# Kernel optimization log

Measured on AMD Instinct MI355X. Metric: run time of the kernel, lower is better.

Reference implementation:

```python
import math
import jax, jax.numpy as jnp
import numpy as np

B, L, DM, D, C = 8, 2048, 512, 512, 2
K_TOP = int(math.floor(C * math.log(L)))  # floor(c * log L) = 15


def setup_inputs() -> dict:
    key = jax.random.key(0)
    ks = jax.random.split(key, 9)
    s = 0.02
    return {
        "Q": jax.random.normal(ks[0], (B, L, DM), jnp.float32),
        "K": jax.random.normal(ks[1], (B, L, DM), jnp.float32),
        "V": jax.random.normal(ks[2], (B, L, DM), jnp.float32),
        "WQ_w": jax.random.normal(ks[3], (DM, D), jnp.float32) * s,
        "WQ_b": jnp.zeros((D,), jnp.float32),
        "WK_w": jax.random.normal(ks[4], (DM, D), jnp.float32) * s,
        "WK_b": jnp.zeros((D,), jnp.float32),
        "WV_w": jax.random.normal(ks[5], (DM, D), jnp.float32) * s,
        "WV_b": jnp.zeros((D,), jnp.float32),
    }


def reference(Q, K, V, WQ_w, WQ_b, WK_w, WK_b, WV_w, WV_b):
    Bn, Ln, _ = Q.shape
    # K/V truncated (zero-padded if shorter) to length L; here S == L.
    Kc = K[:, :Ln, :]
    Vc = V[:, :Ln, :]
    # Dense projections
    q = Q @ WQ_w + WQ_b    # [B, L, d]
    k = Kc @ WK_w + WK_b   # [B, L, d]
    v = Vc @ WV_w + WV_b   # [B, L, d]
    # FFT-based autocorrelation along the time axis
    Qf = jnp.fft.rfft(q, axis=1)
    Kf = jnp.fft.rfft(k, axis=1)
    Rxx = jnp.fft.irfft(Qf * jnp.conjugate(Kf), n=Ln, axis=1)  # [B, L, d]
    # Top-k lag selection per (batch, channel)
    Rl = jnp.moveaxis(Rxx, 1, -1)                # [B, d, L]
    Wk, Ik = jax.lax.top_k(Rl, K_TOP)            # [B, d, k]
    Wk = jax.nn.softmax(Wk, axis=-1)
    # Weighted aggregation of time-rolled values: roll(v, -i)[t] = v[(t+i) % L]
    vl = jnp.moveaxis(v, 1, -1)                  # [B, d, L]
    t = jnp.arange(Ln)
    idx = (t[None, None, None, :] + Ik[..., None]) % Ln   # [B, d, k, L]
    rolled = jnp.take_along_axis(vl[:, :, None, :], idx, axis=-1)  # [B, d, k, L]
    A = jnp.einsum('bdk,bdkl->bld', Wk, rolled)  # [B, L, d]
    return A
```

## Files before the change

kernel.cpp:

```cpp
#include <hip/hip_runtime.h>
#include <hip/hip_bf16.h>
#include <math.h>

#define Bz 8
#define Lz 2048
#define Dz 512
#define KTOP 15

typedef __attribute__((ext_vector_type(8))) unsigned short ushort8x;
typedef __attribute__((ext_vector_type(8))) _Float16 half8x;
typedef __attribute__((ext_vector_type(4))) float floatx4;
typedef __attribute__((ext_vector_type(16))) float float16x;

__global__ __launch_bounds__(256) void wtrans3(
    const float* __restrict__ w0, const float* __restrict__ w1,
    const float* __restrict__ w2, _Float16* __restrict__ t0,
    _Float16* __restrict__ t1, _Float16* __restrict__ t2) {
  const float* w = blockIdx.z == 0 ? w0 : (blockIdx.z == 1 ? w1 : w2);
  _Float16* t = blockIdx.z == 0 ? t0 : (blockIdx.z == 1 ? t1 : t2);
  __shared__ float tile[32][33];
  const int n0 = blockIdx.x * 32, k0 = blockIdx.y * 32;
  const int tx = threadIdx.x, ty = threadIdx.y;
  #pragma unroll
  for (int i = 0; i < 4; ++i)
    tile[ty + 8 * i][tx] = w[(size_t)(k0 + ty + 8 * i) * Dz + n0 + tx];
  __syncthreads();
  #pragma unroll
  for (int i = 0; i < 4; ++i)
    t[(size_t)(n0 + ty + 8 * i) * Dz + k0 + tx] = (_Float16)tile[tx][ty + 8 * i];
}

#define GLDA 40
__global__ __launch_bounds__(256) void gemm3(
    const float* __restrict__ A0, const float* __restrict__ A1,
    const float* __restrict__ A2, const _Float16* __restrict__ B0,
    const _Float16* __restrict__ B1, const _Float16* __restrict__ B2,
    const float* __restrict__ c0, const float* __restrict__ c1,
    const float* __restrict__ c2, _Float16* __restrict__ o0,
    _Float16* __restrict__ o1, _Float16* __restrict__ o2) {
  const int K = Dz;
  const int z = blockIdx.z;
  const float* A = z == 0 ? A0 : (z == 1 ? A1 : A2);
  const _Float16* Bt = z == 0 ? B0 : (z == 1 ? B1 : B2);
  const float* bias = z == 0 ? c0 : (z == 1 ? c1 : c2);
  _Float16* oT = z == 0 ? o0 : (z == 1 ? o1 : o2);

  __shared__ _Float16 smem[20480];
  _Float16* Asb = smem;
  _Float16* Bsb = smem + 10240;
  const int tid = threadIdx.x;
  const int m0 = blockIdx.y * 128;
  const int n0 = blockIdx.x * 128;
  const int lane = tid & 63;
  const int wv = tid >> 6;
  const int wr = wv & 1, wc = wv >> 1;
  const int ln = lane & 15;
  const int quad = lane >> 4;

  floatx4 acc[4][4];
  #pragma unroll
  for (int i = 0; i < 4; ++i)
    #pragma unroll
    for (int j = 0; j < 4; ++j) acc[i][j] = (floatx4){0.f, 0.f, 0.f, 0.f};

  float4 ra4[4];
  ushort8x rb[2];

  #pragma unroll
  for (int j = 0; j < 4; ++j) {
    const int slot = tid + 256 * j;
    const int r = slot >> 3, c4 = slot & 7;
    ra4[j] = *(const float4*)&A[(size_t)(m0 + r) * K + 4 * c4];
  }
  #pragma unroll
  for (int j = 0; j < 2; ++j) {
    const int slot = tid + 256 * j;
    const int r = slot >> 2, ch = slot & 3;
    rb[j] = *(const ushort8x*)((const unsigned short*)Bt +
                               (size_t)(n0 + r) * K + 8 * ch);
  }
  {
    _Float16* As = Asb;
    _Float16* Bs = Bsb;
    #pragma unroll
    for (int j = 0; j < 4; ++j) {
      const int slot = tid + 256 * j;
      const int r = slot >> 3, c4 = slot & 7;
      union { _Float16 h[4]; unsigned long long u; } p;
      p.h[0] = (_Float16)ra4[j].x;
      p.h[1] = (_Float16)ra4[j].y;
      p.h[2] = (_Float16)ra4[j].z;
      p.h[3] = (_Float16)ra4[j].w;
      *(unsigned long long*)&As[r * GLDA + 4 * c4] = p.u;
    }
    #pragma unroll
    for (int j = 0; j < 2; ++j) {
      const int slot = tid + 256 * j;
      const int r = slot >> 2, ch = slot & 3;
      *(ushort8x*)&Bs[r * GLDA + 8 * ch] = rb[j];
    }
  }
  __syncthreads();

  const int NKT = K / 32;
  for (int kt = 0; kt < NKT; ++kt) {
    const int cur = kt & 1;
    if (kt + 1 < NKT) {
      const int kof = (kt + 1) * 32;
      #pragma unroll
      for (int j = 0; j < 4; ++j) {
        const int slot = tid + 256 * j;
        const int r = slot >> 3, c4 = slot & 7;
        ra4[j] = *(const float4*)&A[(size_t)(m0 + r) * K + kof + 4 * c4];
      }
      #pragma unroll
      for (int j = 0; j < 2; ++j) {
        const int slot = tid + 256 * j;
        const int r = slot >> 2, ch = slot & 3;
        rb[j] = *(const ushort8x*)((const unsigned short*)Bt +
                                   (size_t)(n0 + r) * K + kof + 8 * ch);
      }
    }
    const _Float16* As = Asb + cur * 5120;
    const _Float16* Bs = Bsb + cur * 5120;
    half8x af[4], bf[4];
    #pragma unroll
    for (int i = 0; i < 4; ++i)
      af[i] = *(const half8x*)&As[(wr * 64 + 16 * i + ln) * GLDA + 8 * quad];
    #pragma unroll
    for (int j = 0; j < 4; ++j)
      bf[j] = *(const half8x*)&Bs[(wc * 64 + 16 * j + ln) * GLDA + 8 * quad];
    #pragma unroll
    for (int i = 0; i < 4; ++i)
      #pragma unroll
      for (int j = 0; j < 4; ++j)
        acc[i][j] = __builtin_amdgcn_mfma_f32_16x16x32_f16(af[i], bf[j], acc[i][j], 0, 0, 0);
    if (kt + 1 < NKT) {
      const int nxt = cur ^ 1;
      _Float16* Asw = Asb + nxt * 5120;
      _Float16* Bsw = Bsb + nxt * 5120;
      #pragma unroll
      for (int j = 0; j < 4; ++j) {
        const int slot = tid + 256 * j;
        const int r = slot >> 3, c4 = slot & 7;
        union { _Float16 h[4]; unsigned long long u; } p;
        p.h[0] = (_Float16)ra4[j].x;
        p.h[1] = (_Float16)ra4[j].y;
        p.h[2] = (_Float16)ra4[j].z;
        p.h[3] = (_Float16)ra4[j].w;
        *(unsigned long long*)&Asw[r * GLDA + 4 * c4] = p.u;
      }
      #pragma unroll
      for (int j = 0; j < 2; ++j) {
        const int slot = tid + 256 * j;
        const int r = slot >> 2, ch = slot & 3;
        *(ushort8x*)&Bsw[r * GLDA + 8 * ch] = rb[j];
      }
      __syncthreads();
    }
  }

  __syncthreads();
  _Float16* TB = smem;
  #pragma unroll
  for (int j = 0; j < 4; ++j) {
    const int n_l = wc * 64 + 16 * j + ln;
    const float bv = bias[n0 + n_l];
    #pragma unroll
    for (int i = 0; i < 4; ++i) {
      const int m_l = wr * 64 + 16 * i + 4 * quad;
      union { _Float16 h[4]; unsigned long long u; } p;
      #pragma unroll
      for (int r = 0; r < 4; ++r) p.h[r] = (_Float16)(acc[i][j][r] + bv);
      *(unsigned long long*)&TB[n_l * 136 + m_l] = p.u;
    }
  }
  __syncthreads();
  const int b = m0 >> 11;
  const int l0 = m0 & 2047;
  #pragma unroll
  for (int it = 0; it < 8; ++it) {
    const int s = tid + 256 * it;
    const int n = s >> 4, c = s & 15;
    *(ushort8x*)(oT + ((size_t)(b * Dz + n0 + n)) * Lz + l0 + 8 * c) =
        *(const ushort8x*)&TB[n * 136 + 8 * c];
  }
}

#define QXS 2072

__device__ __forceinline__ int swz128(int byte) {
  return byte ^ (((byte >> 7) & 7) << 4);
}

__global__ __launch_bounds__(256) void corr_mfma_topk(
    const _Float16* __restrict__ qT, const _Float16* __restrict__ kT,
    float* __restrict__ Wk, int* __restrict__ Ik) {
  __shared__ __attribute__((aligned(16))) unsigned short qx[8 * QXS];
  __shared__ __attribute__((aligned(16))) unsigned short ke[Lz];
  __shared__ float cv[64];
  __shared__ int ci[64];

  const int tid = threadIdx.x;
  const size_t chan = (size_t)blockIdx.x * Lz;
  const unsigned short* qg = (const unsigned short*)(qT + chan);
  const unsigned short* kg = (const unsigned short*)(kT + chan);

  {
    ushort8x v = *(const ushort8x*)(kg + 8 * tid);
    *(ushort8x*)((char*)ke + swz128(16 * tid)) = v;
  }
  for (int c = tid; c < QXS / 8; c += 256) {
    union { unsigned int d[8]; ushort8x v[2]; } b;
    b.v[0] = *(const ushort8x*)(qg + ((8 * c) & (Lz - 1)));
    b.v[1] = *(const ushort8x*)(qg + ((8 * c + 8) & (Lz - 1)));
    #pragma unroll
    for (int s = 0; s < 8; ++s) {
      union { unsigned int d[4]; ushort8x v; } w;
      if (s & 1) {
        #pragma unroll
        for (int t = 0; t < 4; ++t)
          w.d[t] = __builtin_amdgcn_alignbit(b.d[(s >> 1) + t + 1],
                                             b.d[(s >> 1) + t], 16);
      } else {
        #pragma unroll
        for (int t = 0; t < 4; ++t) w.d[t] = b.d[(s >> 1) + t];
      }
      *(ushort8x*)&qx[s * QXS + 8 * c] = w.v;
    }
  }
  __syncthreads();

  const int lane = tid & 63;
  const int wv = tid >> 6;
  const int jb = lane & 31;
  const int hi = lane >> 5;
  const char* aptr = (const char*)qx + (jb & 7) * (2 * QXS) + 16 * (jb >> 3) + 16 * hi;
  const int bb2 = ((8 * hi - 32 * jb) & (Lz - 1)) * 2;

  float16x acc0 = {0.f, 0.f, 0.f, 0.f, 0.f, 0.f, 0.f, 0.f,
                   0.f, 0.f, 0.f, 0.f, 0.f, 0.f, 0.f, 0.f};
  float16x acc1 = acc0;

  const int t0base = wv << 9;
  #pragma unroll 4
  for (int it = 0; it < 32; ++it) {
    const int t2 = 2 * (t0base + 16 * it);
    half8x a = *(const half8x*)(aptr + t2);
    const int y0 = (bb2 + t2) & (2 * Lz - 1);
    const int y1 = (y0 + 2048) & (2 * Lz - 1);
    half8x b0 = *(const half8x*)((const char*)ke + swz128(y0));
    half8x b1 = *(const half8x*)((const char*)ke + swz128(y1));
    acc0 = __builtin_amdgcn_mfma_f32_32x32x16_f16(a, b0, acc0, 0, 0, 0);
    acc1 = __builtin_amdgcn_mfma_f32_32x32x16_f16(a, b1, acc1, 0, 0, 0);
  }

  __syncthreads();
  float* red = (float*)qx;
  {
    const int rbase = wv * 8192;
    #pragma unroll
    for (int g = 0; g < 4; ++g) {
      const int tau0 = 8 * g + 4 * hi + 32 * jb;
      float4 p0, p1;
      p0.x = acc0[4 * g + 0]; p0.y = acc0[4 * g + 1];
      p0.z = acc0[4 * g + 2]; p0.w = acc0[4 * g + 3];
      p1.x = acc1[4 * g + 0]; p1.y = acc1[4 * g + 1];
      p1.z = acc1[4 * g + 2]; p1.w = acc1[4 * g + 3];
      *(float4*)((char*)red + swz128(rbase + 4 * tau0)) = p0;
      *(float4*)((char*)red + swz128(rbase + 4 * (tau0 + 1024))) = p1;
    }
  }
  __syncthreads();

  float vals[8] = {0.f, 0.f, 0.f, 0.f, 0.f, 0.f, 0.f, 0.f};
  {
    const char* rb = (const char*)red;
    #pragma unroll
    for (int w = 0; w < 4; ++w) {
      float4 a0 = *(const float4*)(rb + swz128(w * 8192 + 32 * tid));
      float4 a1 = *(const float4*)(rb + swz128(w * 8192 + 32 * tid + 16));
      vals[0] += a0.x; vals[1] += a0.y; vals[2] += a0.z; vals[3] += a0.w;
      vals[4] += a1.x; vals[5] += a1.y; vals[6] += a1.z; vals[7] += a1.w;
    }
  }

  unsigned key[8];
  #pragma unroll
  for (int j = 0; j < 8; ++j) {
    const unsigned u = __float_as_uint(vals[j]);
    key[j] = u ^ (unsigned)(((int)u >> 31) | 0x80000000);
  }
  unsigned p = 0;
  for (int b = 31; b >= 0; --b) {
    const unsigned c = p | (1u << b);
    int cnt = 0;
    #pragma unroll
    for (int j = 0; j < 8; ++j)
      cnt += __popcll(__ballot(key[j] >= c));
    if (cnt >= KTOP) p = c;
  }
  const unsigned long long ltm = (1ull << lane) - 1ull;
  int base = 0;
  #pragma unroll
  for (int j = 0; j < 8; ++j) {
    const bool g = key[j] > p;
    const unsigned long long m = __ballot(g);
    const int pos = base + __popcll(m & ltm);
    if (g) { cv[wv * KTOP + pos] = vals[j]; ci[wv * KTOP + pos] = 8 * tid + j; }
    base += __popcll(m);
  }
  #pragma unroll
  for (int j = 0; j < 8; ++j) {
    const bool e = (key[j] == p);
    const unsigned long long m = __ballot(e);
    const int pos = base + __popcll(m & ltm);
    if (e && pos < KTOP) { cv[wv * KTOP + pos] = vals[j]; ci[wv * KTOP + pos] = 8 * tid + j; }
    base += __popcll(m);
  }
  __syncthreads();

  if (wv == 0) {
    const bool act = lane < 4 * KTOP;
    const float v = act ? cv[lane] : 0.f;
    const int ti = act ? ci[lane] : 0;
    unsigned k2 = 0;
    if (act) {
      const unsigned u = __float_as_uint(v);
      k2 = u ^ (unsigned)(((int)u >> 31) | 0x80000000);
    }
    unsigned pp = 0;
    for (int b = 31; b >= 0; --b) {
      const unsigned c = pp | (1u << b);
      if (__popcll(__ballot(k2 >= c)) >= KTOP) pp = c;
    }
    const unsigned long long mg = __ballot(k2 > pp);
    const int tot = __popcll(mg);
    bool sel = (k2 > pp);
    int pos = __popcll(mg & ltm);
    const unsigned long long me = __ballot(k2 == pp);
    const int pose = tot + __popcll(me & ltm);
    if (k2 == pp && pose < KTOP) { sel = true; pos = pose; }
    if (sel) { cv[pos] = v; ci[pos] = ti; }
    const float sv = (lane < KTOP) ? cv[lane] : -3.0e38f;
    const int si = (lane < KTOP) ? ci[lane] : 0;
    float gm = sv;
    #pragma unroll
    for (int off = 1; off < 64; off <<= 1)
      gm = fmaxf(gm, __shfl_xor(gm, off, 64));
    float e = (lane < KTOP) ? expf(sv - gm) : 0.f;
    float es = e;
    #pragma unroll
    for (int off = 1; off < 64; off <<= 1) es += __shfl_xor(es, off, 64);
    if (lane < KTOP) {
      const size_t ob = (size_t)blockIdx.x * KTOP;
      Wk[ob + lane] = e / es;
      Ik[ob + lane] = si;
    }
  }
}

#define GSWZ(b) ((b) ^ ((((b) >> 12) & 7) << 4))

__global__ __launch_bounds__(256) void gather_fused(
    const _Float16* __restrict__ vT, const float* __restrict__ Wk,
    const int* __restrict__ Ik, float* __restrict__ out) {
  __shared__ __attribute__((aligned(16))) _Float16 ls[8 * Lz];
  __shared__ float os[256 * 9];
  const int tid = threadIdx.x;
  const int d0 = blockIdx.x * 8;
  const int b = blockIdx.y;
  float* ob = out + (size_t)b * Lz * Dz;

  const char* lsb = (const char*)ls;
  #pragma unroll
  for (int it = 0; it < 8; ++it) {
    const int slot = tid + 256 * it;
    const int dl2 = slot >> 8, c = slot & 255;
    ushort8x v = *(const ushort8x*)((const unsigned short*)vT +
                                    ((size_t)(b * Dz + d0 + dl2) * Lz) + 8 * c);
    *(ushort8x*)((char*)ls + GSWZ(16 * slot)) = v;
  }

  const int dl = tid & 7;
  const int lg = tid >> 3;
  const size_t wb = ((size_t)b * Dz + d0 + dl) * KTOP;
  float wreg[KTOP];
  int ireg[KTOP];
  #pragma unroll
  for (int k = 0; k < KTOP; ++k) {
    wreg[k] = Wk[wb + k];
    ireg[k] = Ik[wb + k];
  }
  __syncthreads();

  const int rowb = dl * 4096;
  for (int lt = 0; lt < 8; ++lt) {
    const int lbase = lt * 256 + lg * 8;
    float acc[8] = {0.f, 0.f, 0.f, 0.f, 0.f, 0.f, 0.f, 0.f};
    for (int k = 0; k < KTOP; ++k) {
      const float w = wreg[k];
      const int p = (lbase + ireg[k]) & (Lz - 1);
      const int b0 = p >> 3;
      const int b1 = (b0 + 1) & 255;
      union { ushort8x v; unsigned d[4]; } A0, A1;
      A0.v = *(const ushort8x*)(lsb + GSWZ(rowb + 16 * b0));
      A1.v = *(const ushort8x*)(lsb + GSWZ(rowb + 16 * b1));
      const int h = p & 7;
      unsigned e0, e1, e2, e3, e4, e5;
      if (h & 4) { e0 = A0.d[2]; e1 = A0.d[3]; e2 = A1.d[0]; e3 = A1.d[1]; e4 = A1.d[2]; e5 = A1.d[3]; }
      else       { e0 = A0.d[0]; e1 = A0.d[1]; e2 = A0.d[2]; e3 = A0.d[3]; e4 = A1.d[0]; e5 = A1.d[1]; }
      unsigned f0, f1, f2, f3, f4;
      if (h & 2) { f0 = e1; f1 = e2; f2 = e3; f3 = e4; f4 = e5; }
      else       { f0 = e0; f1 = e1; f2 = e2; f3 = e3; f4 = e4; }
      const int sh = (h & 1) << 4;
      unsigned o0 = __builtin_amdgcn_alignbit(f1, f0, sh);
      unsigned o1 = __builtin_amdgcn_alignbit(f2, f1, sh);
      unsigned o2 = __builtin_amdgcn_alignbit(f3, f2, sh);
      unsigned o3 = __builtin_amdgcn_alignbit(f4, f3, sh);
      union { unsigned u; _Float16 hh[2]; } c0, c1, c2, c3;
      c0.u = o0; c1.u = o1; c2.u = o2; c3.u = o3;
      acc[0] += w * (float)c0.hh[0]; acc[1] += w * (float)c0.hh[1];
      acc[2] += w * (float)c1.hh[0]; acc[3] += w * (float)c1.hh[1];
      acc[4] += w * (float)c2.hh[0]; acc[5] += w * (float)c2.hh[1];
      acc[6] += w * (float)c3.hh[0]; acc[7] += w * (float)c3.hh[1];
    }
    __syncthreads();
    #pragma unroll
    for (int j = 0; j < 8; ++j) os[(lg * 8 + j) * 9 + dl] = acc[j];
    __syncthreads();
    #pragma unroll
    for (int c2 = 0; c2 < 2; ++c2) {
      const int sl = tid + 256 * c2;
      const int l = sl >> 1, c = sl & 1;
      float4 o;
      o.x = os[l * 9 + 4 * c + 0];
      o.y = os[l * 9 + 4 * c + 1];
      o.z = os[l * 9 + 4 * c + 2];
      o.w = os[l * 9 + 4 * c + 3];
      *(float4*)&ob[(size_t)(lt * 256 + l) * Dz + d0 + 4 * c] = o;
    }
  }
}

extern "C" void kernel_launch(void* const* d_in, const int* in_sizes, int n_in,
                              void* d_out, int out_size, void* d_ws, size_t ws_size,
                              hipStream_t stream) {
  const float* Q = (const float*)d_in[0];
  const float* K = (const float*)d_in[1];
  const float* V = (const float*)d_in[2];
  const float* WQw = (const float*)d_in[3];
  const float* WQb = (const float*)d_in[4];
  const float* WKw = (const float*)d_in[5];
  const float* WKb = (const float*)d_in[6];
  const float* WVw = (const float*)d_in[7];
  const float* WVb = (const float*)d_in[8];
  float* out = (float*)d_out;

  const size_t CH = (size_t)Bz * Dz;
  const size_t NEL = (size_t)Bz * Lz * Dz;

  char* ws = (char*)d_ws;
  _Float16* qT = (_Float16*)ws;
  _Float16* kT = qT + NEL;
  _Float16* vT = kT + NEL;
  _Float16* WQt = vT + NEL;
  _Float16* WKt = WQt + (size_t)Dz * Dz;
  _Float16* WVt = WKt + (size_t)Dz * Dz;
  float* Wk = (float*)(WVt + (size_t)Dz * Dz);
  int* Ik = (int*)(Wk + CH * KTOP);

  dim3 tr_block(32, 8);

  wtrans3<<<dim3(16, 16, 3), tr_block, 0, stream>>>(WQw, WKw, WVw, WQt, WKt, WVt);

  gemm3<<<dim3(Dz / 128, (Bz * Lz) / 128, 3), dim3(256), 0, stream>>>(
      Q, K, V, WQt, WKt, WVt, WQb, WKb, WVb, qT, kT, vT);

  corr_mfma_topk<<<dim3((unsigned)CH), dim3(256), 0, stream>>>(qT, kT, Wk, Ik);

  gather_fused<<<dim3(Dz / 8, Bz), dim3(256), 0, stream>>>(vT, Wk, Ik, out);
}
```

Baseline: 269.1 us.

## Load GEMM B tiles directly into LDS and drop LDS-staged epilogue

The projection GEMM now fetches the fp16 transposed weight tiles with global_load_lds into an unpadded, XOR-swizzled LDS layout. This removes the register round trip and the separate LDS stores for B, and shrinks shared memory. The epilogue no longer transposes through LDS with extra barriers. Each lane now writes 8-byte fp16 chunks straight to the transposed output, which saves LDS traffic and syncs but makes the global writes narrower and less coalesced.

After: 272.1 us. About the same (+1.1%).

```diff
diff --git a/kernel.cpp b/kernel.cpp
--- a/kernel.cpp
+++ b/kernel.cpp
@@ -30,7 +30,7 @@
     t[(size_t)(n0 + ty + 8 * i) * Dz + k0 + tx] = (_Float16)tile[tx][ty + 8 * i];
 }
 
-#define GLDA 40
+#define ALDA 40
 __global__ __launch_bounds__(256) void gemm3(
     const float* __restrict__ A0, const float* __restrict__ A1,
     const float* __restrict__ A2, const _Float16* __restrict__ B0,
@@ -45,7 +45,7 @@
   const float* bias = z == 0 ? c0 : (z == 1 ? c1 : c2);
   _Float16* oT = z == 0 ? o0 : (z == 1 ? o1 : o2);
 
-  __shared__ _Float16 smem[20480];
+  __shared__ __attribute__((aligned(16))) _Float16 smem[18432];
   _Float16* Asb = smem;
   _Float16* Bsb = smem + 10240;
   const int tid = threadIdx.x;
@@ -64,7 +64,6 @@
     for (int j = 0; j < 4; ++j) acc[i][j] = (floatx4){0.f, 0.f, 0.f, 0.f};
 
   float4 ra4[4];
-  ushort8x rb[2];
 
   #pragma unroll
   for (int j = 0; j < 4; ++j) {
@@ -73,38 +72,34 @@
     ra4[j] = *(const float4*)&A[(size_t)(m0 + r) * K + 4 * c4];
   }
   #pragma unroll
-  for (int j = 0; j < 2; ++j) {
+  for (int jj = 0; jj < 2; ++jj) {
+    const int s = tid + 256 * jj;
+    const int row = s >> 2;
+    const int qs = (s & 3) ^ (row & 3);
+    const unsigned short* src =
+        (const unsigned short*)Bt + (size_t)(n0 + row) * K + 8 * qs;
+    __builtin_amdgcn_global_load_lds(
+        (const __attribute__((address_space(1))) unsigned int*)src,
+        (__attribute__((address_space(3))) unsigned int*)&Bsb[(jj * 256 + wv * 64) * 8],
+        16, 0, 0);
+  }
+  #pragma unroll
+  for (int j = 0; j < 4; ++j) {
     const int slot = tid + 256 * j;
-    const int r = slot >> 2, ch = slot & 3;
-    rb[j] = *(const ushort8x*)((const unsigned short*)Bt +
-                               (size_t)(n0 + r) * K + 8 * ch);
-  }
-  {
-    _Float16* As = Asb;
-    _Float16* Bs = Bsb;
-    #pragma unroll
-    for (int j = 0; j < 4; ++j) {
-      const int slot = tid + 256 * j;
-      const int r = slot >> 3, c4 = slot & 7;
-      union { _Float16 h[4]; unsigned long long u; } p;
-      p.h[0] = (_Float16)ra4[j].x;
-      p.h[1] = (_Float16)ra4[j].y;
-      p.h[2] = (_Float16)ra4[j].z;
-      p.h[3] = (_Float16)ra4[j].w;
-      *(unsigned long long*)&As[r * GLDA + 4 * c4] = p.u;
-    }
-    #pragma unroll
-    for (int j = 0; j < 2; ++j) {
-      const int slot = tid + 256 * j;
-      const int r = slot >> 2, ch = slot & 3;
-      *(ushort8x*)&Bs[r * GLDA + 8 * ch] = rb[j];
-    }
+    const int r = slot >> 3, c4 = slot & 7;
+    union { _Float16 h[4]; unsigned long long u; } p;
+    p.h[0] = (_Float16)ra4[j].x;
+    p.h[1] = (_Float16)ra4[j].y;
+    p.h[2] = (_Float16)ra4[j].z;
+    p.h[3] = (_Float16)ra4[j].w;
+    *(unsigned long long*)&Asb[r * ALDA + 4 * c4] = p.u;
   }
   __syncthreads();
 
   const int NKT = K / 32;
   for (int kt = 0; kt < NKT; ++kt) {
     const int cur = kt & 1;
+    const int nxt = cur ^ 1;
     if (kt + 1 < NKT) {
       const int kof = (kt + 1) * 32;
       #pragma unroll
@@ -114,31 +109,37 @@
         ra4[j] = *(const float4*)&A[(size_t)(m0 + r) * K + kof + 4 * c4];
       }
       #pragma unroll
-      for (int j = 0; j < 2; ++j) {
-        const int slot = tid + 256 * j;
-        const int r = slot >> 2, ch = slot & 3;
-        rb[j] = *(const ushort8x*)((const unsigned short*)Bt +
-                                   (size_t)(n0 + r) * K + kof + 8 * ch);
+      for (int jj = 0; jj < 2; ++jj) {
+        const int s = tid + 256 * jj;
+        const int row = s >> 2;
+        const int qs = (s & 3) ^ (row & 3);
+        const unsigned short* src =
+            (const unsigned short*)Bt + (size_t)(n0 + row) * K + kof + 8 * qs;
+        __builtin_amdgcn_global_load_lds(
+            (const __attribute__((address_space(1))) unsigned int*)src,
+            (__attribute__((address_space(3))) unsigned int*)
+                &Bsb[nxt * 4096 + (jj * 256 + wv * 64) * 8],
+            16, 0, 0);
       }
     }
     const _Float16* As = Asb + cur * 5120;
-    const _Float16* Bs = Bsb + cur * 5120;
+    const _Float16* Bs = Bsb + cur * 4096;
     half8x af[4], bf[4];
     #pragma unroll
     for (int i = 0; i < 4; ++i)
-      af[i] = *(const half8x*)&As[(wr * 64 + 16 * i + ln) * GLDA + 8 * quad];
-    #pragma unroll
-    for (int j = 0; j < 4; ++j)
-      bf[j] = *(const half8x*)&Bs[(wc * 64 + 16 * j + ln) * GLDA + 8 * quad];
+      af[i] = *(const half8x*)&As[(wr * 64 + 16 * i + ln) * ALDA + 8 * quad];
+    #pragma unroll
+    for (int j = 0; j < 4; ++j) {
+      const int row = wc * 64 + 16 * j + ln;
+      bf[j] = *(const half8x*)&Bs[row * 32 + 8 * (quad ^ (ln & 3))];
+    }
     #pragma unroll
     for (int i = 0; i < 4; ++i)
       #pragma unroll
       for (int j = 0; j < 4; ++j)
         acc[i][j] = __builtin_amdgcn_mfma_f32_16x16x32_f16(af[i], bf[j], acc[i][j], 0, 0, 0);
     if (kt + 1 < NKT) {
-      const int nxt = cur ^ 1;
       _Float16* Asw = Asb + nxt * 5120;
-      _Float16* Bsw = Bsb + nxt * 5120;
       #pragma unroll
       for (int j = 0; j < 4; ++j) {
         const int slot = tid + 256 * j;
@@ -148,42 +149,26 @@
         p.h[1] = (_Float16)ra4[j].y;
         p.h[2] = (_Float16)ra4[j].z;
         p.h[3] = (_Float16)ra4[j].w;
-        *(unsigned long long*)&Asw[r * GLDA + 4 * c4] = p.u;
-      }
-      #pragma unroll
-      for (int j = 0; j < 2; ++j) {
-        const int slot = tid + 256 * j;
-        const int r = slot >> 2, ch = slot & 3;
-        *(ushort8x*)&Bsw[r * GLDA + 8 * ch] = rb[j];
+        *(unsigned long long*)&Asw[r * ALDA + 4 * c4] = p.u;
       }
       __syncthreads();
     }
   }
 
-  __syncthreads();
-  _Float16* TB = smem;
+  const int bb = m0 >> 11;
+  const int l0 = m0 & 2047;
   #pragma unroll
   for (int j = 0; j < 4; ++j) {
-    const int n_l = wc * 64 + 16 * j + ln;
-    const float bv = bias[n0 + n_l];
+    const int d = n0 + wc * 64 + 16 * j + ln;
+    const float bv = bias[d];
+    _Float16* op = oT + (size_t)(bb * Dz + d) * Lz + l0 + wr * 64 + 4 * quad;
     #pragma unroll
     for (int i = 0; i < 4; ++i) {
-      const int m_l = wr * 64 + 16 * i + 4 * quad;
       union { _Float16 h[4]; unsigned long long u; } p;
       #pragma unroll
       for (int r = 0; r < 4; ++r) p.h[r] = (_Float16)(acc[i][j][r] + bv);
-      *(unsigned long long*)&TB[n_l * 136 + m_l] = p.u;
-    }
-  }
-  __syncthreads();
-  const int b = m0 >> 11;
-  const int l0 = m0 & 2047;
-  #pragma unroll
-  for (int it = 0; it < 8; ++it) {
-    const int s = tid + 256 * it;
-    const int n = s >> 4, c = s & 15;
-    *(ushort8x*)(oT + ((size_t)(b * Dz + n0 + n)) * Lz + l0 + 8 * c) =
-        *(const ushort8x*)&TB[n * 136 + 8 * c];
+      *(unsigned long long*)(op + 16 * i) = p.u;
+    }
   }
 }
 
```

## Deepen gemm3 global-load prefetch to two stages with lightweight barriers

Applied to the files above, without the earlier changes.

The projection GEMM now keeps two K-tiles of global loads in flight in registers, issuing loads for tile kt+2 right after the MFMAs of tile kt. The shared-memory write for tile kt+1 then uses data loaded an iteration earlier. The __syncthreads is replaced with an explicit lgkmcnt wait, sched_barrier and s_barrier. Launch bounds now request 4 waves per SIMD. The aim is to hide global-load latency, at the cost of more live registers, which may spill or cut occupancy under the new bound.

Result: slower. 450.6 us (+67.4%).

```diff
diff --git a/kernel.cpp b/kernel.cpp
--- a/kernel.cpp
+++ b/kernel.cpp
@@ -31,7 +31,7 @@
 }
 
 #define GLDA 40
-__global__ __launch_bounds__(256) void gemm3(
+__global__ __launch_bounds__(256, 4) void gemm3(
     const float* __restrict__ A0, const float* __restrict__ A1,
     const float* __restrict__ A2, const _Float16* __restrict__ B0,
     const _Float16* __restrict__ B1, const _Float16* __restrict__ B2,
@@ -45,7 +45,7 @@
   const float* bias = z == 0 ? c0 : (z == 1 ? c1 : c2);
   _Float16* oT = z == 0 ? o0 : (z == 1 ? o1 : o2);
 
-  __shared__ _Float16 smem[20480];
+  __shared__ __attribute__((aligned(16))) _Float16 smem[20480];
   _Float16* Asb = smem;
   _Float16* Bsb = smem + 10240;
   const int tid = threadIdx.x;
@@ -63,64 +63,59 @@
     #pragma unroll
     for (int j = 0; j < 4; ++j) acc[i][j] = (floatx4){0.f, 0.f, 0.f, 0.f};
 
-  float4 ra4[4];
-  ushort8x rb[2];
-
-  #pragma unroll
-  for (int j = 0; j < 4; ++j) {
-    const int slot = tid + 256 * j;
-    const int r = slot >> 3, c4 = slot & 7;
-    ra4[j] = *(const float4*)&A[(size_t)(m0 + r) * K + 4 * c4];
-  }
-  #pragma unroll
-  for (int j = 0; j < 2; ++j) {
-    const int slot = tid + 256 * j;
-    const int r = slot >> 2, ch = slot & 3;
-    rb[j] = *(const ushort8x*)((const unsigned short*)Bt +
-                               (size_t)(n0 + r) * K + 8 * ch);
-  }
-  {
-    _Float16* As = Asb;
-    _Float16* Bs = Bsb;
-    #pragma unroll
-    for (int j = 0; j < 4; ++j) {
-      const int slot = tid + 256 * j;
-      const int r = slot >> 3, c4 = slot & 7;
-      union { _Float16 h[4]; unsigned long long u; } p;
-      p.h[0] = (_Float16)ra4[j].x;
-      p.h[1] = (_Float16)ra4[j].y;
-      p.h[2] = (_Float16)ra4[j].z;
-      p.h[3] = (_Float16)ra4[j].w;
-      *(unsigned long long*)&As[r * GLDA + 4 * c4] = p.u;
-    }
-    #pragma unroll
-    for (int j = 0; j < 2; ++j) {
-      const int slot = tid + 256 * j;
-      const int r = slot >> 2, ch = slot & 3;
-      *(ushort8x*)&Bs[r * GLDA + 8 * ch] = rb[j];
-    }
-  }
-  __syncthreads();
+  float4 ra[2][4];
+  ushort8x rb[2][2];
+
+#define G_ISSUE(S, KOF)                                                     \
+  {                                                                         \
+    _Pragma("unroll") for (int j = 0; j < 4; ++j) {                         \
+      const int slot = tid + 256 * j;                                       \
+      const int r = slot >> 3, c4 = slot & 7;                               \
+      ra[S][j] = *(const float4*)&A[(size_t)(m0 + r) * K + (KOF) + 4 * c4]; \
+    }                                                                       \
+    _Pragma("unroll") for (int j = 0; j < 2; ++j) {                         \
+      const int slot = tid + 256 * j;                                       \
+      const int r = slot >> 2, ch = slot & 3;                               \
+      rb[S][j] = *(const ushort8x*)((const unsigned short*)Bt +             \
+                                    (size_t)(n0 + r) * K + (KOF) + 8 * ch); \
+    }                                                                       \
+  }
+
+#define G_WRITE(S, ASW, BSW)                                                \
+  {                                                                         \
+    _Pragma("unroll") for (int j = 0; j < 4; ++j) {                         \
+      const int slot = tid + 256 * j;                                       \
+      const int r = slot >> 3, c4 = slot & 7;                               \
+      union { _Float16 h[4]; unsigned long long u; } p;                     \
+      p.h[0] = (_Float16)ra[S][j].x;                                        \
+      p.h[1] = (_Float16)ra[S][j].y;                                        \
+      p.h[2] = (_Float16)ra[S][j].z;                                        \
+      p.h[3] = (_Float16)ra[S][j].w;                                        \
+      *(unsigned long long*)&(ASW)[r * GLDA + 4 * c4] = p.u;                \
+    }                                                                       \
+    _Pragma("unroll") for (int j = 0; j < 2; ++j) {                         \
+      const int slot = tid + 256 * j;                                       \
+      const int r = slot >> 2, ch = slot & 3;                               \
+      *(ushort8x*)&(BSW)[r * GLDA + 8 * ch] = rb[S][j];                     \
+    }                                                                       \
+  }
+
+#define PIPE_BARRIER()                                   \
+  asm volatile("s_waitcnt lgkmcnt(0)" ::: "memory");     \
+  __builtin_amdgcn_sched_barrier(0);                     \
+  __builtin_amdgcn_s_barrier();                          \
+  __builtin_amdgcn_sched_barrier(0);
+
+  G_ISSUE(0, 0);
+  G_ISSUE(1, 32);
+  G_WRITE(0, Asb, Bsb);
+  PIPE_BARRIER();
 
   const int NKT = K / 32;
+  #pragma unroll 2
   for (int kt = 0; kt < NKT; ++kt) {
     const int cur = kt & 1;
-    if (kt + 1 < NKT) {
-      const int kof = (kt + 1) * 32;
-      #pragma unroll
-      for (int j = 0; j < 4; ++j) {
-        const int slot = tid + 256 * j;
-        const int r = slot >> 3, c4 = slot & 7;
-        ra4[j] = *(const float4*)&A[(size_t)(m0 + r) * K + kof + 4 * c4];
-      }
-      #pragma unroll
-      for (int j = 0; j < 2; ++j) {
-        const int slot = tid + 256 * j;
-        const int r = slot >> 2, ch = slot & 3;
-        rb[j] = *(const ushort8x*)((const unsigned short*)Bt +
-                                   (size_t)(n0 + r) * K + kof + 8 * ch);
-      }
-    }
+    const int nxt = cur ^ 1;
     const _Float16* As = Asb + cur * 5120;
     const _Float16* Bs = Bsb + cur * 5120;
     half8x af[4], bf[4];
@@ -135,28 +130,12 @@
       #pragma unroll
       for (int j = 0; j < 4; ++j)
         acc[i][j] = __builtin_amdgcn_mfma_f32_16x16x32_f16(af[i], bf[j], acc[i][j], 0, 0, 0);
+    if (kt + 2 < NKT) {
+      G_ISSUE(cur, (kt + 2) * 32);
+    }
     if (kt + 1 < NKT) {
-      const int nxt = cur ^ 1;
-      _Float16* Asw = Asb + nxt * 5120;
-      _Float16* Bsw = Bsb + nxt * 5120;
-      #pragma unroll
-      for (int j = 0; j < 4; ++j) {
-        const int slot = tid + 256 * j;
-        const int r = slot >> 3, c4 = slot & 7;
-        union { _Float16 h[4]; unsigned long long u; } p;
-        p.h[0] = (_Float16)ra4[j].x;
-        p.h[1] = (_Float16)ra4[j].y;
-        p.h[2] = (_Float16)ra4[j].z;
-        p.h[3] = (_Float16)ra4[j].w;
-        *(unsigned long long*)&Asw[r * GLDA + 4 * c4] = p.u;
-      }
-      #pragma unroll
-      for (int j = 0; j < 2; ++j) {
-        const int slot = tid + 256 * j;
-        const int r = slot >> 2, ch = slot & 3;
-        *(ushort8x*)&Bsw[r * GLDA + 8 * ch] = rb[j];
-      }
-      __syncthreads();
+      G_WRITE(nxt, Asb + nxt * 5120, Bsb + nxt * 5120);
+      PIPE_BARRIER();
     }
   }
 
```
